# Performance work log

Hardware: AMD Instinct MI355X
Metric: run time of the kernel (lower is better)

The kernel has to match this reference:

```python
import jax, jax.numpy as jnp
import numpy as np

TOP_K = 2


def setup_inputs() -> dict:
    key = jax.random.key(0)
    k0, k1, k2, k3 = jax.random.split(key, 4)
    B, T, C, E, D = 4, 2048, 1024, 8, 1024  # D = 4*C*top_k//E
    x = jax.random.normal(k0, (B, T, C), dtype=jnp.float32)
    s = 1.0 / np.sqrt(C)
    w_router = jax.random.normal(k1, (C, E), dtype=jnp.float32) * s
    w1 = jax.random.normal(k2, (E, C, D), dtype=jnp.float32) * s  # c_fc.weight.T per expert
    w2 = jax.random.normal(k3, (E, D, C), dtype=jnp.float32) * (1.0 / np.sqrt(D))  # c_proj.weight.T
    return {"x": x, "w_router": w_router, "w1": w1, "w2": w2}


def reference(x, w_router, w1, w2):
    B, T, C = x.shape
    xf = x.reshape(-1, C)  # [N, C]
    logits = xf @ w_router  # [N, E]
    top_vals, top_idx = jax.lax.top_k(logits, TOP_K)  # [N, k]
    probs = jax.nn.softmax(top_vals, axis=-1)  # softmax over selected experts only
    # Dense per-expert MLP (relu^2), identical math to per-token weight gather:
    h = jnp.square(jax.nn.relu(jnp.einsum('nc,ecd->ned', xf, w1)))  # [N, E, D]
    y_all = jnp.einsum('ned,edc->nec', h, w2)  # [N, E, C]
    y_sel = jnp.take_along_axis(y_all, top_idx[:, :, None], axis=1)  # [N, k, C]
    out = jnp.sum(y_sel * probs[:, :, None], axis=1)  # [N, C]
    return out.reshape(B, T, C)
```

## Files before the change

### kernel.cpp

```cpp
#include <hip/hip_runtime.h>
#include <stdint.h>

typedef unsigned short u16;
typedef unsigned int u32;

constexpr int C = 1024;
constexpr int E = 8;
constexpr int D = 1024;
constexpr int BM = 128, BN = 128, BK = 32;
constexpr int WLS = 1032;

typedef short s16x8 __attribute__((ext_vector_type(8)));
typedef float f32x4 __attribute__((ext_vector_type(4)));

__device__ __forceinline__ u16 f2bf(float f) {
  union { float f; u32 u; } v; v.f = f;
  return (u16)((v.u + 0x7FFFu + ((v.u >> 16) & 1u)) >> 16);
}
__device__ __forceinline__ float bf2f(u32 u) {
  union { u32 u; float f; } v; v.u = u << 16; return v.f;
}

typedef __attribute__((address_space(1))) const u32 gu32;
typedef __attribute__((address_space(3))) u32 lu32;
__device__ __forceinline__ void gl_lds16(const void* g, void* l) {
  __builtin_amdgcn_global_load_lds((gu32*)g, (lu32*)l, 16, 0, 0);
}
template <int N>
__device__ __forceinline__ void waitvm() {
  asm volatile("s_waitcnt vmcnt(%0)" :: "i"(N) : "memory");
  __builtin_amdgcn_sched_barrier(0);
}
__device__ __forceinline__ void bar() {
  __builtin_amdgcn_s_barrier();
  __builtin_amdgcn_sched_barrier(0);
}

__global__ void __launch_bounds__(256) k_prep(const float* __restrict__ x,
                                              const float* __restrict__ wr,
                                              const float* __restrict__ w1,
                                              const float* __restrict__ w2,
                                              u16* __restrict__ xb,
                                              u16* __restrict__ w1t,
                                              u16* __restrict__ w2t,
                                              int* __restrict__ tok_e,
                                              float* __restrict__ tok_p,
                                              int* __restrict__ counts,
                                              int RB) {
  __shared__ __align__(16) float pool[8 * WLS + 32 * 9 + 8];
  int b = blockIdx.x;
  int t = threadIdx.x;
  if (b >= RB) {
    float (*tile)[65] = (float (*)[65])pool;
    int b2 = b - RB;
    int which = b2 >> 11;
    int rem = b2 & 2047;
    int e = rem >> 8, kt = (rem >> 4) & 15, nt = rem & 15;
    const float* src = (which ? w2 : w1) + (size_t)e * C * D;
    u16* dst = (which ? w2t : w1t) + (size_t)e * C * D;
#pragma unroll
    for (int i = 0; i < 4; ++i) {
      int lin = i * 256 + t;
      int r = lin >> 4, c4 = lin & 15;
      f32x4 v = *(const f32x4*)(src + (size_t)(kt * 64 + r) * 1024 + nt * 64 + c4 * 4);
      tile[r][c4 * 4 + 0] = v[0]; tile[r][c4 * 4 + 1] = v[1];
      tile[r][c4 * 4 + 2] = v[2]; tile[r][c4 * 4 + 3] = v[3];
    }
    __syncthreads();
#pragma unroll
    for (int i = 0; i < 2; ++i) {
      int lin = i * 256 + t;
      int nr = lin >> 3, k8 = lin & 7;
      u32 o[4];
#pragma unroll
      for (int j = 0; j < 4; ++j)
        o[j] = (u32)f2bf(tile[k8 * 8 + 2 * j][nr]) |
               ((u32)f2bf(tile[k8 * 8 + 2 * j + 1][nr]) << 16);
      *(uint4*)(dst + (size_t)(nt * 64 + nr) * 1024 + kt * 64 + k8 * 8) = *(const uint4*)o;
    }
    return;
  }
  float* wl = pool;
  float (*lg)[9] = (float (*)[9])(pool + 8 * WLS);
  int* cl = (int*)(pool + 8 * WLS + 32 * 9);
  for (int i = t; i < 2048; i += 256) {
    f32x4 v = ((const f32x4*)wr)[i];
    int c0 = i >> 1, e0 = (i & 1) << 2;
    wl[(e0 + 0) * WLS + c0] = v[0]; wl[(e0 + 1) * WLS + c0] = v[1];
    wl[(e0 + 2) * WLS + c0] = v[2]; wl[(e0 + 3) * WLS + c0] = v[3];
  }
  if (t < 8) cl[t] = 0;
  __syncthreads();
  int tok0 = b * 32;
  int tl = t >> 3, e = t & 7;
  size_t tok = (size_t)tok0 + tl;
  const f32x4* xr = (const f32x4*)(x + tok * C);
  const f32x4* wv4 = (const f32x4*)&wl[e * WLS];
  float a0 = 0.f, a1 = 0.f, a2 = 0.f, a3 = 0.f;
#pragma unroll 4
  for (int i = 0; i < C / 4; ++i) {
    f32x4 xv = xr[i], wv = wv4[i];
    a0 += xv[0] * wv[0]; a1 += xv[1] * wv[1];
    a2 += xv[2] * wv[2]; a3 += xv[3] * wv[3];
  }
  lg[tl][e] = (a0 + a1) + (a2 + a3);
  __syncthreads();
  if (t < 32) {
    int myTok = tok0 + t;
    float v0 = -1e30f; int i0 = 0;
#pragma unroll
    for (int q = 0; q < 8; ++q) { float v = lg[t][q]; if (v > v0) { v0 = v; i0 = q; } }
    float v1 = -1e30f; int i1 = 0;
#pragma unroll
    for (int q = 0; q < 8; ++q) {
      if (q == i0) continue;
      float v = lg[t][q]; if (v > v1) { v1 = v; i1 = q; }
    }
    float dd = expf(v1 - v0);
    float s = 1.f / (1.f + dd);
    tok_e[myTok * 2 + 0] = i0; tok_e[myTok * 2 + 1] = i1;
    tok_p[myTok * 2 + 0] = s;  tok_p[myTok * 2 + 1] = dd * s;
    atomicAdd(&cl[i0], 1); atomicAdd(&cl[i1], 1);
  }
  __syncthreads();
  if (t < 8 && cl[t] > 0) atomicAdd(&counts[t], cl[t]);
  const f32x4* xall = (const f32x4*)(x + (size_t)tok0 * C);
  uint2* xb2 = (uint2*)(xb + (size_t)tok0 * C);
  for (int i = t; i < 32 * C / 4; i += 256) {
    f32x4 v = xall[i];
    uint2 o;
    o.x = (u32)f2bf(v[0]) | ((u32)f2bf(v[1]) << 16);
    o.y = (u32)f2bf(v[2]) | ((u32)f2bf(v[3]) << 16);
    xb2[i] = o;
  }
}

__global__ void __launch_bounds__(256) k_build(const int* __restrict__ tok_e,
                                               const int* __restrict__ counts,
                                               int* __restrict__ cnt2,
                                               int* __restrict__ offs,
                                               int* __restrict__ list_tok,
                                               int* __restrict__ inv) {
  int gid = blockIdx.x * 256 + threadIdx.x;
  int offv[9]; int off = 0;
#pragma unroll
  for (int q = 0; q < 8; ++q) { offv[q] = off; off += (counts[q] + (BM - 1)) & ~(BM - 1); }
  offv[8] = off;
  if (blockIdx.x == 0 && threadIdx.x < 9) offs[threadIdx.x] = offv[threadIdx.x];
  int lane = threadIdx.x & 63;
#pragma unroll
  for (int s = 0; s < 2; ++s) {
    int e = tok_e[gid * 2 + s];
    for (int q = 0; q < 8; ++q) {
      unsigned long long mask = __ballot(e == q);
      if (mask == 0ull) continue;
      int leader = __ffsll(mask) - 1;
      int cnt = __popcll(mask);
      int base = 0;
      if (lane == leader) base = atomicAdd(&cnt2[q], cnt);
      base = __shfl(base, leader, 64);
      if (e == q) {
        int pos = offv[q] + base + __popcll(mask & ((1ull << lane) - 1ull));
        list_tok[pos] = gid;
        inv[gid * 2 + s] = pos;
      }
    }
  }
}

template <int MODE>
__global__ void __launch_bounds__(256, 3) k_gemm(const u16* __restrict__ A,
                                                 const u16* __restrict__ Bt,
                                                 u16* __restrict__ Hout,
                                                 const int* __restrict__ list_tok,
                                                 const int* __restrict__ offs,
                                                 int Ntok) {
  __shared__ u16 A0[BM * BK], B0[BN * BK], A1[BM * BK], B1[BN * BK], A2[BM * BK], B2[BN * BK];
  int b = blockIdx.x;
  int nper = gridDim.x >> 3;
  int logical = (b & 7) * nper + (b >> 3);
  int m0 = (logical >> 3) * BM;
  int n0 = (logical & 7) * BN;
  if (m0 >= offs[8]) return;
  int e = 0;
#pragma unroll
  for (int q = 1; q < 8; ++q) e += (m0 >= offs[q]);

  int t = threadIdx.x;
  int l = t & 63, w = t >> 6;
  int wm = w >> 1, wn = w & 1;

  const u16* ag[2]; const u16* bg[2];
#pragma unroll
  for (int j = 0; j < 2; ++j) {
    int row = w * 32 + j * 16 + (l >> 2);
    int coff = (((l & 3) ^ ((row >> 1) & 3)) << 3);
    if (MODE == 0) {
      int tk = list_tok[m0 + row];
      tk = (tk < 0 || tk >= Ntok) ? 0 : tk;
      ag[j] = A + (size_t)tk * C + coff;
    } else {
      ag[j] = A + (size_t)(m0 + row) * C + coff;
    }
    bg[j] = Bt + (size_t)e * C * D + (size_t)(n0 + row) * 1024 + coff;
  }
  u16* a0 = &A0[w * 1024]; u16* b0 = &B0[w * 1024];
  u16* a1 = &A1[w * 1024]; u16* b1 = &B1[w * 1024];
  u16* a2 = &A2[w * 1024]; u16* b2 = &B2[w * 1024];

  f32x4 acc[4][4];
#pragma unroll
  for (int m = 0; m < 4; ++m)
#pragma unroll
    for (int n = 0; n < 4; ++n) acc[m][n] = (f32x4){0.f, 0.f, 0.f, 0.f};

  auto STAGE = [&](int k0, u16* al, u16* bl) {
#pragma unroll
    for (int j = 0; j < 2; ++j) {
      gl_lds16(ag[j] + k0, al + j * 512);
      gl_lds16(bg[j] + k0, bl + j * 512);
    }
  };
  auto COMPUTE = [&](const u16* Al, const u16* Bl) {
    s16x8 af[4], bf[4];
    int cr = l >> 4;
#pragma unroll
    for (int m = 0; m < 4; ++m) {
      int row = wm * 64 + m * 16 + (l & 15);
      af[m] = *(const s16x8*)&Al[row * BK + ((cr ^ ((row >> 1) & 3)) << 3)];
    }
#pragma unroll
    for (int n = 0; n < 4; ++n) {
      int row = wn * 64 + n * 16 + (l & 15);
      bf[n] = *(const s16x8*)&Bl[row * BK + ((cr ^ ((row >> 1) & 3)) << 3)];
    }
    __builtin_amdgcn_s_setprio(1);
#pragma unroll
    for (int m = 0; m < 4; ++m)
#pragma unroll
      for (int n = 0; n < 4; ++n)
        acc[m][n] = __builtin_amdgcn_mfma_f32_16x16x32_bf16(af[m], bf[n], acc[m][n], 0, 0, 0);
    __builtin_amdgcn_s_setprio(0);
  };

  STAGE(0, a0, b0);
  STAGE(BK, a1, b1);
#pragma unroll 1
  for (int tt = 0; tt < 30; tt += 3) {
    STAGE((tt + 2) * BK, a2, b2); waitvm<8>(); bar(); COMPUTE(A0, B0); bar();
    STAGE((tt + 3) * BK, a0, b0); waitvm<8>(); bar(); COMPUTE(A1, B1); bar();
    STAGE((tt + 4) * BK, a1, b1); waitvm<8>(); bar(); COMPUTE(A2, B2); bar();
  }
  waitvm<4>(); bar(); COMPUTE(A0, B0);
  waitvm<0>(); bar(); COMPUTE(A1, B1);

#pragma unroll
  for (int m = 0; m < 4; ++m) {
#pragma unroll
    for (int r = 0; r < 4; ++r) {
      int grow = m0 + wm * 64 + m * 16 + ((l >> 4) << 2) + r;
      u16* hp = Hout + (size_t)grow * 1024 + n0 + wn * 64 + (l & 15);
#pragma unroll
      for (int n = 0; n < 4; ++n) {
        float v = acc[m][n][r];
        if (MODE == 0) { v = fmaxf(v, 0.f); v = v * v; }
        hp[n * 16] = f2bf(v);
      }
    }
  }
}

__global__ void __launch_bounds__(256) k_combine(const u16* __restrict__ Y,
                                                 const int* __restrict__ inv,
                                                 const float* __restrict__ tok_p,
                                                 float* __restrict__ out) {
  int gid = blockIdx.x * 4 + (threadIdx.x >> 6);
  int l = threadIdx.x & 63;
  int s0 = inv[gid * 2 + 0], s1 = inv[gid * 2 + 1];
  float p0 = tok_p[gid * 2 + 0], p1 = tok_p[gid * 2 + 1];
  const uint4* y0 = (const uint4*)(Y + (size_t)s0 * 1024);
  const uint4* y1 = (const uint4*)(Y + (size_t)s1 * 1024);
  f32x4* o = (f32x4*)(out + (size_t)gid * 1024);
#pragma unroll
  for (int i = 0; i < 2; ++i) {
    int c = i * 64 + l;
    uint4 a = y0[c], bb = y1[c];
    f32x4 r0, r1;
    r0[0] = p0 * bf2f(a.x & 0xffffu) + p1 * bf2f(bb.x & 0xffffu);
    r0[1] = p0 * bf2f(a.x >> 16)     + p1 * bf2f(bb.x >> 16);
    r0[2] = p0 * bf2f(a.y & 0xffffu) + p1 * bf2f(bb.y & 0xffffu);
    r0[3] = p0 * bf2f(a.y >> 16)     + p1 * bf2f(bb.y >> 16);
    r1[0] = p0 * bf2f(a.z & 0xffffu) + p1 * bf2f(bb.z & 0xffffu);
    r1[1] = p0 * bf2f(a.z >> 16)     + p1 * bf2f(bb.z >> 16);
    r1[2] = p0 * bf2f(a.w & 0xffffu) + p1 * bf2f(bb.w & 0xffffu);
    r1[3] = p0 * bf2f(a.w >> 16)     + p1 * bf2f(bb.w >> 16);
    o[c * 2 + 0] = r0;
    o[c * 2 + 1] = r1;
  }
}

extern "C" void kernel_launch(void* const* d_in, const int* in_sizes, int n_in,
                              void* d_out, int out_size, void* d_ws, size_t ws_size,
                              hipStream_t stream) {
  const float* x  = (const float*)d_in[0];
  const float* wr = (const float*)d_in[1];
  const float* w1 = (const float*)d_in[2];
  const float* w2 = (const float*)d_in[3];
  float* out = (float*)d_out;
  const int Ntok = in_sizes[0] / C;
  const int ROWS = 2 * Ntok + E * BM;
  const int G = (ROWS / BM) * 8;
  const int RB = Ntok / 32;

  char* p = (char*)d_ws;
  u16* xb  = (u16*)p; p += (size_t)Ntok * C * 2;
  u16* w1t = (u16*)p; p += (size_t)E * C * D * 2;
  u16* w2t = (u16*)p; p += (size_t)E * C * D * 2;
  u16* h   = (u16*)p; p += (size_t)ROWS * D * 2;
  u16* y   = (u16*)p; p += (size_t)ROWS * C * 2;
  int* list_tok = (int*)p; p += (size_t)ROWS * 4;
  int* inv = (int*)p; p += (size_t)Ntok * 2 * 4;
  int* tok_e = (int*)p; p += (size_t)Ntok * 2 * 4;
  float* tok_p = (float*)p; p += (size_t)Ntok * 2 * 4;
  int* ints = (int*)p; p += 256;
  int* counts = ints;
  int* offs = ints + 16;
  int* cnt2 = ints + 32;
  (void)ws_size; (void)n_in; (void)out_size;

  hipMemsetAsync(ints, 0, 256, stream);
  k_prep<<<RB + 4096, 256, 0, stream>>>(x, wr, w1, w2, xb, w1t, w2t, tok_e, tok_p, counts, RB);
  k_build<<<Ntok / 256, 256, 0, stream>>>(tok_e, counts, cnt2, offs, list_tok, inv);
  k_gemm<0><<<G, 256, 0, stream>>>(xb, w1t, h, list_tok, offs, Ntok);
  k_gemm<1><<<G, 256, 0, stream>>>(h, w2t, y, list_tok, offs, Ntok);
  k_combine<<<Ntok / 4, 256, 0, stream>>>(y, inv, tok_p, out);
}
```

Before: 182.1 us.

## Fuse router logits with bf16 cast using coalesced wave-per-row reduction

Result: faster. 170.5 us (-6.4%).

```diff
diff --git a/kernel.cpp b/kernel.cpp
--- a/kernel.cpp
+++ b/kernel.cpp
@@ -47,7 +47,7 @@
                                               float* __restrict__ tok_p,
                                               int* __restrict__ counts,
                                               int RB) {
-  __shared__ __align__(16) float pool[8 * WLS + 32 * 9 + 8];
+  __shared__ __align__(16) float pool[8 * WLS + 32];
   int b = blockIdx.x;
   int t = threadIdx.x;
   if (b >= RB) {
@@ -81,8 +81,7 @@
     return;
   }
   float* wl = pool;
-  float (*lg)[9] = (float (*)[9])(pool + 8 * WLS);
-  int* cl = (int*)(pool + 8 * WLS + 32 * 9);
+  int* cl = (int*)(pool + 8 * WLS);
   for (int i = t; i < 2048; i += 256) {
     f32x4 v = ((const f32x4*)wr)[i];
     int c0 = i >> 1, e0 = (i & 1) << 2;
@@ -92,47 +91,52 @@
   if (t < 8) cl[t] = 0;
   __syncthreads();
   int tok0 = b * 32;
-  int tl = t >> 3, e = t & 7;
-  size_t tok = (size_t)tok0 + tl;
-  const f32x4* xr = (const f32x4*)(x + tok * C);
-  const f32x4* wv4 = (const f32x4*)&wl[e * WLS];
-  float a0 = 0.f, a1 = 0.f, a2 = 0.f, a3 = 0.f;
-#pragma unroll 4
-  for (int i = 0; i < C / 4; ++i) {
-    f32x4 xv = xr[i], wv = wv4[i];
-    a0 += xv[0] * wv[0]; a1 += xv[1] * wv[1];
-    a2 += xv[2] * wv[2]; a3 += xv[3] * wv[3];
-  }
-  lg[tl][e] = (a0 + a1) + (a2 + a3);
-  __syncthreads();
-  if (t < 32) {
-    int myTok = tok0 + t;
-    float v0 = -1e30f; int i0 = 0;
-#pragma unroll
-    for (int q = 0; q < 8; ++q) { float v = lg[t][q]; if (v > v0) { v0 = v; i0 = q; } }
-    float v1 = -1e30f; int i1 = 0;
-#pragma unroll
-    for (int q = 0; q < 8; ++q) {
-      if (q == i0) continue;
-      float v = lg[t][q]; if (v > v1) { v1 = v; i1 = q; }
-    }
-    float dd = expf(v1 - v0);
-    float s = 1.f / (1.f + dd);
-    tok_e[myTok * 2 + 0] = i0; tok_e[myTok * 2 + 1] = i1;
-    tok_p[myTok * 2 + 0] = s;  tok_p[myTok * 2 + 1] = dd * s;
-    atomicAdd(&cl[i0], 1); atomicAdd(&cl[i1], 1);
+  int l = t & 63, w = t >> 6;
+#pragma unroll 1
+  for (int rr = 0; rr < 8; ++rr) {
+    int row = tok0 + w * 8 + rr;
+    const f32x4* xr = (const f32x4*)(x + (size_t)row * C);
+    uint2* xb2 = (uint2*)(xb + (size_t)row * C);
+    float acc[8];
+#pragma unroll
+    for (int e = 0; e < 8; ++e) acc[e] = 0.f;
+#pragma unroll
+    for (int it = 0; it < 4; ++it) {
+      int c4 = it * 64 + l;
+      f32x4 xv = xr[c4];
+      uint2 o;
+      o.x = (u32)f2bf(xv[0]) | ((u32)f2bf(xv[1]) << 16);
+      o.y = (u32)f2bf(xv[2]) | ((u32)f2bf(xv[3]) << 16);
+      xb2[c4] = o;
+#pragma unroll
+      for (int e = 0; e < 8; ++e) {
+        f32x4 wv = *(const f32x4*)&wl[e * WLS + c4 * 4];
+        acc[e] += xv[0] * wv[0] + xv[1] * wv[1] + xv[2] * wv[2] + xv[3] * wv[3];
+      }
+    }
+#pragma unroll
+    for (int off = 1; off < 64; off <<= 1)
+#pragma unroll
+      for (int e = 0; e < 8; ++e) acc[e] += __shfl_xor(acc[e], off, 64);
+    if (l == 0) {
+      float v0 = -1e30f; int i0 = 0;
+#pragma unroll
+      for (int q = 0; q < 8; ++q) { if (acc[q] > v0) { v0 = acc[q]; i0 = q; } }
+      float v1 = -1e30f; int i1 = 0;
+#pragma unroll
+      for (int q = 0; q < 8; ++q) {
+        if (q == i0) continue;
+        if (acc[q] > v1) { v1 = acc[q]; i1 = q; }
+      }
+      float dd = expf(v1 - v0);
+      float s = 1.f / (1.f + dd);
+      tok_e[row * 2 + 0] = i0; tok_e[row * 2 + 1] = i1;
+      tok_p[row * 2 + 0] = s;  tok_p[row * 2 + 1] = dd * s;
+      atomicAdd(&cl[i0], 1); atomicAdd(&cl[i1], 1);
+    }
   }
   __syncthreads();
   if (t < 8 && cl[t] > 0) atomicAdd(&counts[t], cl[t]);
-  const f32x4* xall = (const f32x4*)(x + (size_t)tok0 * C);
-  uint2* xb2 = (uint2*)(xb + (size_t)tok0 * C);
-  for (int i = t; i < 32 * C / 4; i += 256) {
-    f32x4 v = xall[i];
-    uint2 o;
-    o.x = (u32)f2bf(v[0]) | ((u32)f2bf(v[1]) << 16);
-    o.y = (u32)f2bf(v[2]) | ((u32)f2bf(v[3]) << 16);
-    xb2[i] = o;
-  }
 }
 
 __global__ void __launch_bounds__(256) k_build(const int* __restrict__ tok_e,
```
